# Optimization experiments

Hardware: AMD Instinct MI355X
Metric: run time of the kernel (lower is better)

The kernel has to match this reference:

```python
import jax, jax.numpy as jnp
import numpy as np
import math

# model / graph sizes
N_NODES, N_EDGES = 50000, 400000
IN_DIM, N_HID = 256, 128
NUM_TYPES, NUM_REL = 4, 5
N_HEADS, D_K = 4, 32
N_LAYERS, MAX_LEN = 2, 240
SQRT_DK = math.sqrt(D_K)


def _gelu(x):
    return jax.nn.gelu(x, approximate=False)  # torch F.gelu is exact erf


def _per_type_linear(x, types, W, b):
    # x:[n,din], types:[n] int, W:[T,din,dout], b:[T,dout]
    out = jnp.zeros((x.shape[0], W.shape[-1]), x.dtype)
    for t in range(W.shape[0]):  # small fixed type count
        out = jnp.where((types == t)[:, None], x @ W[t] + b[t], out)
    return out


def setup_inputs() -> dict:
    key = jax.random.key(0)
    ks = jax.random.split(key, 16)
    node_feature = jax.random.normal(ks[0], (N_NODES, IN_DIM), jnp.float32)
    node_type = jax.random.randint(ks[1], (N_NODES,), 0, NUM_TYPES)
    edge_index = jax.random.randint(ks[2], (2, N_EDGES), 0, N_NODES)
    edge_type = jax.random.randint(ks[3], (N_EDGES,), 0, NUM_REL)
    edge_time = jax.random.randint(ks[4], (N_EDGES,), 0, MAX_LEN)

    def w(k, shape, s=0.05):
        return jax.random.normal(k, shape, jnp.float32) * s

    adapt_W = w(ks[5], (NUM_TYPES, IN_DIM, N_HID))
    adapt_b = jnp.zeros((NUM_TYPES, N_HID), jnp.float32)
    Wk = w(ks[6], (N_LAYERS, NUM_TYPES, N_HID, N_HID))
    Wq = w(ks[7], (N_LAYERS, NUM_TYPES, N_HID, N_HID))
    Wv = w(ks[8], (N_LAYERS, NUM_TYPES, N_HID, N_HID))
    Wa = w(ks[9], (N_LAYERS, NUM_TYPES, N_HID, N_HID))
    bk = jnp.zeros((N_LAYERS, NUM_TYPES, N_HID), jnp.float32)
    bq = jnp.zeros((N_LAYERS, NUM_TYPES, N_HID), jnp.float32)
    bv = jnp.zeros((N_LAYERS, NUM_TYPES, N_HID), jnp.float32)
    ba = jnp.zeros((N_LAYERS, NUM_TYPES, N_HID), jnp.float32)
    rel_pri = jnp.ones((N_LAYERS, NUM_REL, N_HEADS), jnp.float32)
    rel_att = w(ks[10], (N_LAYERS, NUM_REL, N_HEADS, D_K, D_K), 0.1) + jnp.eye(D_K, dtype=jnp.float32)
    rel_msg = w(ks[11], (N_LAYERS, NUM_REL, N_HEADS, D_K, D_K), 0.1) + jnp.eye(D_K, dtype=jnp.float32)
    skip = jnp.ones((N_LAYERS, NUM_TYPES), jnp.float32)
    # fixed sinusoidal RTE table (pyHGT RelTemporalEncoding, requires_grad=False)
    pos = np.arange(MAX_LEN, dtype=np.float32)[:, None]
    div = np.exp(np.arange(0, N_HID, 2, dtype=np.float32) * -(math.log(10000.0) / N_HID))
    tab = np.zeros((MAX_LEN, N_HID), np.float32)
    tab[:, 0::2] = np.sin(pos * div) / math.sqrt(N_HID)
    tab[:, 1::2] = np.cos(pos * div) / math.sqrt(N_HID)
    rte_emb = jnp.asarray(tab)
    rte_W = w(ks[12], (N_LAYERS, N_HID, N_HID))
    rte_b = jnp.zeros((N_LAYERS, N_HID), jnp.float32)
    return dict(node_feature=node_feature, adapt_W=adapt_W, adapt_b=adapt_b,
                Wk=Wk, bk=bk, Wq=Wq, bq=bq, Wv=Wv, bv=bv, Wa=Wa, ba=ba,
                rel_pri=rel_pri, rel_att=rel_att, rel_msg=rel_msg, skip=skip,
                rte_emb=rte_emb, rte_W=rte_W, rte_b=rte_b,
                node_type=node_type, edge_index=edge_index,
                edge_type=edge_type, edge_time=edge_time)


def reference(node_feature, adapt_W, adapt_b, Wk, bk, Wq, bq, Wv, bv, Wa, ba,
              rel_pri, rel_att, rel_msg, skip, rte_emb, rte_W, rte_b,
              node_type, edge_index, edge_type, edge_time):
    n = node_feature.shape[0]
    src, dst = edge_index[0], edge_index[1]  # PyG: row0 = source j, row1 = target i
    st, tt = node_type[src], node_type[dst]
    # per-type input adaptation (all types use Linear + GELU)
    h = _gelu(_per_type_linear(node_feature, node_type, adapt_W, adapt_b))  # [N, n_hid]
    for l in range(N_LAYERS):  # HGTConv stack
        x_j, x_i = h[src], h[dst]
        s_e = x_j + rte_emb[edge_time] @ rte_W[l] + rte_b[l]  # RTE on source per edge
        k = _per_type_linear(s_e, st, Wk[l], bk[l]).reshape(-1, N_HEADS, D_K)
        v = _per_type_linear(s_e, st, Wv[l], bv[l]).reshape(-1, N_HEADS, D_K)
        q = _per_type_linear(x_i, tt, Wq[l], bq[l]).reshape(-1, N_HEADS, D_K)
        att = jnp.zeros((k.shape[0], N_HEADS), h.dtype)
        msg = jnp.zeros_like(v)
        for r in range(NUM_REL):  # small fixed relation count
            m = edge_type == r
            kr = jnp.einsum('ehd,hdk->ehk', k, rel_att[l, r])
            ar = jnp.einsum('ehd,ehd->eh', q, kr) * rel_pri[l, r] / SQRT_DK
            mr = jnp.einsum('ehd,hdk->ehk', v, rel_msg[l, r])
            att = jnp.where(m[:, None], ar, att)
            msg = jnp.where(m[:, None, None], mr, msg)
        # segment softmax over incoming edges of each target node
        amax = jax.lax.stop_gradient(jax.ops.segment_max(att, dst, num_segments=n))
        ex = jnp.exp(att - amax[dst])
        denom = jax.ops.segment_sum(ex, dst, num_segments=n)
        alpha = ex / (denom[dst] + 1e-16)
        aggr = jax.ops.segment_sum((msg * alpha[:, :, None]).reshape(-1, N_HEADS * D_K),
                                   dst, num_segments=n)  # [N, n_hid]
        g = _gelu(aggr)
        res = jnp.zeros_like(h)
        for t in range(NUM_TYPES):  # per-type output transform + gated skip
            a_t = jax.nn.sigmoid(skip[l, t])
            res = jnp.where((node_type == t)[:, None],
                            (g @ Wa[l, t] + ba[l, t]) * a_t + h * (1.0 - a_t), res)
        h = res
    return h
```

## Files before the change

### kernel.cpp

```cpp
#include <hip/hip_runtime.h>
#include <math.h>

#define NN     50000
#define NE     400000
#define INDIM  256
#define NH     128
#define NTYPE  4
#define NREL   5
#define NHEAD  4
#define DK     32
#define RSQRT_DK 0.17677669529663687f
#define BN     64
#define NSCAN_BLK ((NN + 255) / 256)
#define XB     260

__device__ __forceinline__ float gelu_f(float x){
    return 0.5f * x * (1.0f + erff(x * 0.70710678118654752f));
}

__global__ void GNN_nscatter(const int* __restrict__ ntype, int* __restrict__ ncur,
                             int* __restrict__ nperm){
    __shared__ int lcnt[4], lbase[4];
    int tid = threadIdx.x;
    if (tid < 4) lcnt[tid] = 0;
    __syncthreads();
    int n = blockIdx.x * 256 + tid;
    int t = 0, lpos = 0;
    bool ok = (n < NN);
    if (ok){ t = ntype[n]; lpos = atomicAdd(&lcnt[t], 1); }
    __syncthreads();
    if (tid < 4 && lcnt[tid] > 0) lbase[tid] = atomicAdd(&ncur[tid], lcnt[tid]);
    __syncthreads();
    if (ok) nperm[t * NN + lbase[t] + lpos] = n;
}

__global__ void GNN_deg(const int* __restrict__ edst, int* __restrict__ deg){
    int e = blockIdx.x * 256 + threadIdx.x;
    if (e < NE) atomicAdd(&deg[edst[e]], 1);
}

__global__ void GNN_scan1(const int* __restrict__ deg, int* __restrict__ rowptr,
                          int* __restrict__ bsum){
    __shared__ int s[256];
    int g = blockIdx.x * 256 + threadIdx.x;
    int v = (g < NN) ? deg[g] : 0;
    s[threadIdx.x] = v;
    __syncthreads();
    for (int off = 1; off < 256; off <<= 1){
        int t = (threadIdx.x >= off) ? s[threadIdx.x - off] : 0;
        __syncthreads();
        s[threadIdx.x] += t;
        __syncthreads();
    }
    if (g < NN) rowptr[g] = s[threadIdx.x] - v;
    if (threadIdx.x == 255) bsum[blockIdx.x] = s[255];
}

__global__ void GNN_scan2(const int* __restrict__ bsum, int* __restrict__ bbase){
    __shared__ int s[256];
    int v = (threadIdx.x < NSCAN_BLK) ? bsum[threadIdx.x] : 0;
    s[threadIdx.x] = v;
    __syncthreads();
    for (int off = 1; off < 256; off <<= 1){
        int t = (threadIdx.x >= off) ? s[threadIdx.x - off] : 0;
        __syncthreads();
        s[threadIdx.x] += t;
        __syncthreads();
    }
    bbase[threadIdx.x] = s[threadIdx.x] - v;
}

__global__ void GNN_scan3(int* __restrict__ rowptr, const int* __restrict__ bbase){
    int g = blockIdx.x * 256 + threadIdx.x;
    if (g < NN) rowptr[g] += bbase[blockIdx.x];
    if (g == 0) rowptr[NN] = NE;
}

__global__ void GNN_csr_scatter(const int* __restrict__ edst, const int* __restrict__ rowptr,
                                int* __restrict__ cursor, int* __restrict__ csr_e){
    int e = blockIdx.x * 256 + threadIdx.x;
    if (e >= NE) return;
    int d = edst[e];
    int pos = atomicAdd(&cursor[d], 1);
    csr_e[rowptr[d] + pos] = e;
}

template<int MODE>
__device__ __forceinline__ void gemm_tile(
    const float* __restrict__ X, int K,
    const float* __restrict__ W, const float* __restrict__ brow,
    float a_t, const float* __restrict__ Hprev,
    float* Xs, float* Ws, const int* nids,
    float* __restrict__ OUT)
{
    int tid = threadIdx.x;
    int cq = tid & 31, rq = tid >> 5;
    float acc[8][4];
    #pragma unroll
    for (int i = 0; i < 8; i++){ acc[i][0]=0.f; acc[i][1]=0.f; acc[i][2]=0.f; acc[i][3]=0.f; }

    for (int k0 = 0; k0 < K; k0 += 32){
        #pragma unroll
        for (int j = 0; j < 2; j++){
            int slot = j * 256 + tid;
            int c4 = slot >> 6, row = slot & 63;
            int nid = nids[row];
            float4 xv = make_float4(0.f, 0.f, 0.f, 0.f);
            if (nid >= 0) xv = *(const float4*)(X + (size_t)nid * K + k0 + c4 * 4);
            *(float4*)&Xs[c4 * XB + row * 4] = xv;
        }
        #pragma unroll
        for (int j = 0; j < 4; j++){
            int slot = j * 256 + tid;
            int kk = slot >> 5, col4 = slot & 31;
            *(float4*)&Ws[kk * 128 + col4 * 4] =
                *(const float4*)(W + (size_t)(k0 + kk) * NH + col4 * 4);
        }
        __syncthreads();
        #pragma unroll 2
        for (int c4 = 0; c4 < 8; c4++){
            float4 w0 = *(const float4*)&Ws[(c4*4+0)*128 + cq*4];
            float4 w1 = *(const float4*)&Ws[(c4*4+1)*128 + cq*4];
            float4 w2 = *(const float4*)&Ws[(c4*4+2)*128 + cq*4];
            float4 w3 = *(const float4*)&Ws[(c4*4+3)*128 + cq*4];
            #pragma unroll
            for (int i = 0; i < 8; i++){
                float4 xv = *(const float4*)&Xs[c4 * XB + (rq + 8*i) * 4];
                acc[i][0] += xv.x*w0.x + xv.y*w1.x + xv.z*w2.x + xv.w*w3.x;
                acc[i][1] += xv.x*w0.y + xv.y*w1.y + xv.z*w2.y + xv.w*w3.y;
                acc[i][2] += xv.x*w0.z + xv.y*w1.z + xv.z*w2.z + xv.w*w3.z;
                acc[i][3] += xv.x*w0.w + xv.y*w1.w + xv.z*w2.w + xv.w*w3.w;
            }
        }
        __syncthreads();
    }

    float4 b4 = *(const float4*)(brow + cq * 4);
    float one_m = 1.f - a_t;
    #pragma unroll
    for (int i = 0; i < 8; i++){
        int r = rq + 8*i;
        int nid = nids[r];
        if (nid < 0) continue;
        float v0 = acc[i][0] + b4.x, v1 = acc[i][1] + b4.y;
        float v2 = acc[i][2] + b4.z, v3 = acc[i][3] + b4.w;
        if (MODE == 0){ v0 = gelu_f(v0); v1 = gelu_f(v1); v2 = gelu_f(v2); v3 = gelu_f(v3); }
        if (MODE == 2){
            float4 hp = *(const float4*)(Hprev + (size_t)nid * NH + cq * 4);
            v0 = v0 * a_t + hp.x * one_m; v1 = v1 * a_t + hp.y * one_m;
            v2 = v2 * a_t + hp.z * one_m; v3 = v3 * a_t + hp.w * one_m;
        }
        *(float4*)(OUT + (size_t)nid * NH + cq * 4) = make_float4(v0, v1, v2, v3);
    }
}

template<int MODE>
__global__ __launch_bounds__(256) void GNN_ptype_gemm(
    const float* __restrict__ X, int K,
    const float* __restrict__ Wall, const float* __restrict__ ball,
    const float* __restrict__ skiprow, const float* __restrict__ Hprev,
    const int* __restrict__ nperm, const int* __restrict__ counts,
    float* __restrict__ OUT)
{
    int t = blockIdx.y;
    int cnt = counts[t];
    int rbase = blockIdx.x * BN;
    if (rbase >= cnt) return;
    __shared__ float Xs[8 * XB];
    __shared__ float Ws[32 * 128];
    __shared__ int nids[BN];
    int tid = threadIdx.x;
    if (tid < BN){
        int idx = rbase + tid;
        nids[tid] = (idx < cnt) ? nperm[t * NN + idx] : -1;
    }
    __syncthreads();
    float a_t = 0.f;
    if (MODE == 2) a_t = 1.f / (1.f + expf(-skiprow[t]));
    gemm_tile<MODE>(X, K, Wall + (size_t)t * K * NH, ball + t * NH,
                    a_t, Hprev, Xs, Ws, nids, OUT);
}

__global__ __launch_bounds__(256) void GNN_qkv_gemm(
    const float* __restrict__ X,
    const float* __restrict__ Wq, const float* __restrict__ bq,
    const float* __restrict__ Wk, const float* __restrict__ bk,
    const float* __restrict__ Wv, const float* __restrict__ bv,
    const int* __restrict__ nperm, const int* __restrict__ counts,
    float* __restrict__ Qn, float* __restrict__ Kn, float* __restrict__ Vn)
{
    int t = blockIdx.y;
    int cnt = counts[t];
    int rbase = blockIdx.x * BN;
    if (rbase >= cnt) return;
    __shared__ float Xs[8 * XB];
    __shared__ float Ws[32 * 128];
    __shared__ int nids[BN];
    int tid = threadIdx.x;
    if (tid < BN){
        int idx = rbase + tid;
        nids[tid] = (idx < cnt) ? nperm[t * NN + idx] : -1;
    }
    __syncthreads();
    int z = blockIdx.z;
    const float* W = (z == 0) ? Wq : (z == 1) ? Wk : Wv;
    const float* b = (z == 0) ? bq : (z == 1) ? bk : bv;
    float* OUT     = (z == 0) ? Qn : (z == 1) ? Kn : Vn;
    gemm_tile<1>(X, NH, W + (size_t)t * NH * NH, b + t * NH,
                 0.f, nullptr, Xs, Ws, nids, OUT);
}

__global__ void GNN_rte_tab(const float* __restrict__ rte_emb, const float* __restrict__ rW,
                            const float* __restrict__ rb, float* __restrict__ tab){
    int m = blockIdx.x, j = threadIdx.x;
    __shared__ float e[NH];
    e[j] = rte_emb[m * NH + j];
    __syncthreads();
    float a = rb[j];
    #pragma unroll 8
    for (int d = 0; d < NH; d++) a += e[d] * rW[d * NH + j];
    tab[m * NH + j] = a;
}

__global__ void GNN_rte_proj(const float* __restrict__ tab, const float* __restrict__ WkL,
                             const float* __restrict__ WvL, float* __restrict__ RK,
                             float* __restrict__ RV){
    int m = blockIdx.x, j = threadIdx.x;
    int sel = blockIdx.y; int t = sel >> 1; int which = sel & 1;
    const float* W = (which ? WvL : WkL) + (size_t)t * NH * NH;
    float* O = which ? RV : RK;
    __shared__ float e[NH];
    e[j] = tab[m * NH + j];
    __syncthreads();
    float a = 0.f;
    #pragma unroll 8
    for (int d = 0; d < NH; d++) a += e[d] * W[d * NH + j];
    O[(size_t)(t * 240 + m) * NH + j] = a;
}

__global__ __launch_bounds__(256) void GNN_qa(
    const float* __restrict__ Qn, const float* __restrict__ relA, float* __restrict__ QA)
{
    __shared__ float Atp[4 * 1072];
    int r = blockIdx.y;
    int nb = blockIdx.x * 64;
    int tid = threadIdx.x;
    const float* Ar = relA + (size_t)r * NHEAD * DK * DK;
    for (int x = tid; x < NHEAD * DK * DK; x += 256){
        int hh = x >> 10, rem = x & 1023, dd = rem >> 5, cc = rem & 31;
        Atp[hh * 1072 + (dd >> 2) * 132 + cc * 4 + (dd & 3)] = Ar[x];
    }
    __syncthreads();
    int cq = tid & 31, rq = tid >> 5;
    int h = cq >> 3;
    int abase = h * 1072 + (cq & 7) * 132;
    int rowoff[8];
    #pragma unroll
    for (int i = 0; i < 8; i++){
        int node = nb + rq + 8*i;
        if (node >= NN) node = NN - 1;
        rowoff[i] = node * NH + h * 32;
    }
    float acc[8][4];
    #pragma unroll
    for (int i = 0; i < 8; i++){ acc[i][0]=0.f; acc[i][1]=0.f; acc[i][2]=0.f; acc[i][3]=0.f; }
    #pragma unroll 2
    for (int c4 = 0; c4 < 8; c4++){
        float4 av0 = *(const float4*)&Atp[abase + c4 * 16 + 0];
        float4 av1 = *(const float4*)&Atp[abase + c4 * 16 + 4];
        float4 av2 = *(const float4*)&Atp[abase + c4 * 16 + 8];
        float4 av3 = *(const float4*)&Atp[abase + c4 * 16 + 12];
        #pragma unroll
        for (int i = 0; i < 8; i++){
            float4 qv = *(const float4*)(Qn + rowoff[i] + c4 * 4);
            acc[i][0] += qv.x*av0.x + qv.y*av1.x + qv.z*av2.x + qv.w*av3.x;
            acc[i][1] += qv.x*av0.y + qv.y*av1.y + qv.z*av2.y + qv.w*av3.y;
            acc[i][2] += qv.x*av0.z + qv.y*av1.z + qv.z*av2.z + qv.w*av3.z;
            acc[i][3] += qv.x*av0.w + qv.y*av1.w + qv.z*av2.w + qv.w*av3.w;
        }
    }
    #pragma unroll
    for (int i = 0; i < 8; i++){
        int node = nb + rq + 8*i;
        if (node >= NN) continue;
        *(float4*)(QA + ((size_t)r * NN + node) * NH + cq * 4) =
            make_float4(acc[i][0], acc[i][1], acc[i][2], acc[i][3]);
    }
}

__global__ __launch_bounds__(256) void GNN_edge_att(
    const float* __restrict__ Kn, const float* __restrict__ RK, const float* __restrict__ QA,
    const int* __restrict__ esrc, const int* __restrict__ edst,
    const int* __restrict__ etype, const int* __restrict__ etime,
    const int* __restrict__ ntype, const float* __restrict__ relP,
    float* __restrict__ att)
{
    int tid = threadIdx.x;
    int e = blockIdx.x * 8 + (tid >> 5);
    if (e >= NE) return;
    int lane = tid & 31;
    int s = esrc[e], d = edst[e], r = etype[e], tm = etime[e];
    int st = ntype[s];
    float4 k4 = *(const float4*)(Kn + (size_t)s * NH + lane * 4);
    float4 rk = *(const float4*)(RK + (size_t)(st * 240 + tm) * NH + lane * 4);
    float4 qa = *(const float4*)(QA + ((size_t)r * NN + d) * NH + lane * 4);
    float pv = (k4.x + rk.x) * qa.x + (k4.y + rk.y) * qa.y
             + (k4.z + rk.z) * qa.z + (k4.w + rk.w) * qa.w;
    pv += __shfl_xor(pv, 4);
    pv += __shfl_xor(pv, 2);
    pv += __shfl_xor(pv, 1);
    if ((lane & 7) == 0){
        int head = lane >> 3;
        att[(size_t)e * NHEAD + head] = pv * relP[r * NHEAD + head] * RSQRT_DK;
    }
}

__global__ __launch_bounds__(256) void GNN_node_aggr(
    const float* __restrict__ att, const float* __restrict__ Vn, const float* __restrict__ RV,
    const int* __restrict__ rowptr, const int* __restrict__ csr_e,
    const int* __restrict__ esrc, const int* __restrict__ etype,
    const int* __restrict__ etime, const int* __restrict__ ntype,
    float* __restrict__ P)
{
    int tid = threadIdx.x;
    int i = blockIdx.x * 8 + (tid >> 5);
    if (i >= NN) return;
    int lane = tid & 31;
    int head = lane >> 3;
    int beg = rowptr[i], end = rowptr[i + 1];
    float mx = -3.4e38f;
    for (int k = beg; k < end; k++){
        int e = csr_e[k];
        mx = fmaxf(mx, att[(size_t)e * NHEAD + head]);
    }
    float4 acc[NREL];
    #pragma unroll
    for (int rr = 0; rr < NREL; rr++) acc[rr] = make_float4(0.f, 0.f, 0.f, 0.f);
    float den = 0.f;
    for (int k = beg; k < end; k++){
        int e = csr_e[k];
        int s = esrc[e], r = etype[e], tm = etime[e];
        int st = ntype[s];
        float ex = expf(att[(size_t)e * NHEAD + head] - mx);
        den += ex;
        float4 v4 = *(const float4*)(Vn + (size_t)s * NH + lane * 4);
        float4 rv = *(const float4*)(RV + (size_t)(st * 240 + tm) * NH + lane * 4);
        float vx = v4.x + rv.x, vy = v4.y + rv.y, vz = v4.z + rv.z, vw = v4.w + rv.w;
        #pragma unroll
        for (int rr = 0; rr < NREL; rr++){
            float w = (rr == r) ? ex : 0.f;
            acc[rr].x += w * vx; acc[rr].y += w * vy;
            acc[rr].z += w * vz; acc[rr].w += w * vw;
        }
    }
    float inv = 1.f / (den + 1e-16f);
    #pragma unroll
    for (int rr = 0; rr < NREL; rr++){
        *(float4*)(P + ((size_t)rr * NN + i) * NH + lane * 4) =
            make_float4(acc[rr].x * inv, acc[rr].y * inv, acc[rr].z * inv, acc[rr].w * inv);
    }
}

__global__ __launch_bounds__(256) void GNN_pm(
    const float* __restrict__ P, const float* __restrict__ relM, float* __restrict__ aggr)
{
    __shared__ float Msp[2][4 * 1072];
    int tid = threadIdx.x;
    int nb = blockIdx.x * 64;
    int cq = tid & 31, rq = tid >> 5;
    int h = cq >> 3;
    int mbase = h * 1072 + (cq & 7) * 132;
    int rowoff[8];
    #pragma unroll
    for (int i = 0; i < 8; i++){
        int node = nb + rq + 8*i;
        if (node >= NN) node = NN - 1;
        rowoff[i] = node * NH + h * 32;
    }
    float acc[8][4];
    #pragma unroll
    for (int i = 0; i < 8; i++){ acc[i][0]=0.f; acc[i][1]=0.f; acc[i][2]=0.f; acc[i][3]=0.f; }

    #pragma unroll
    for (int j = 0; j < 4; j++){
        int s = tid + 256 * j;
        float4 mv = *(const float4*)(relM + 4 * s);
        *(float4*)&Msp[0][(s >> 8) * 1072 + (s & 7) * 132 + ((s >> 3) & 31) * 4] = mv;
    }
    __syncthreads();

    #pragma unroll
    for (int r = 0; r < NREL; r++){
        float4 mpre[4];
        if (r + 1 < NREL){
            const float* Mn = relM + (size_t)(r + 1) * NHEAD * DK * DK;
            #pragma unroll
            for (int j = 0; j < 4; j++)
                mpre[j] = *(const float4*)(Mn + 4 * (tid + 256 * j));
        }
        const float* Ms = Msp[r & 1];
        const float* Pr = P + (size_t)r * NN * NH;
        #pragma unroll 2
        for (int d4 = 0; d4 < 8; d4++){
            float4 mv0 = *(const float4*)&Ms[mbase + d4 * 16 + 0];
            float4 mv1 = *(const float4*)&Ms[mbase + d4 * 16 + 4];
            float4 mv2 = *(const float4*)&Ms[mbase + d4 * 16 + 8];
            float4 mv3 = *(const float4*)&Ms[mbase + d4 * 16 + 12];
            #pragma unroll
            for (int i = 0; i < 8; i++){
                float4 pv = *(const float4*)(Pr + rowoff[i] + d4 * 4);
                acc[i][0] += pv.x*mv0.x + pv.y*mv1.x + pv.z*mv2.x + pv.w*mv3.x;
                acc[i][1] += pv.x*mv0.y + pv.y*mv1.y + pv.z*mv2.y + pv.w*mv3.y;
                acc[i][2] += pv.x*mv0.z + pv.y*mv1.z + pv.z*mv2.z + pv.w*mv3.z;
                acc[i][3] += pv.x*mv0.w + pv.y*mv1.w + pv.z*mv2.w + pv.w*mv3.w;
            }
        }
        if (r + 1 < NREL){
            #pragma unroll
            for (int j = 0; j < 4; j++){
                int s = tid + 256 * j;
                *(float4*)&Msp[(r + 1) & 1][(s >> 8) * 1072 + (s & 7) * 132 +
                                            ((s >> 3) & 31) * 4] = mpre[j];
            }
            __syncthreads();
        }
    }
    #pragma unroll
    for (int i = 0; i < 8; i++){
        int node = nb + rq + 8*i;
        if (node >= NN) continue;
        *(float4*)(aggr + (size_t)node * NH + cq * 4) =
            make_float4(gelu_f(acc[i][0]), gelu_f(acc[i][1]),
                        gelu_f(acc[i][2]), gelu_f(acc[i][3]));
    }
}

extern "C" void kernel_launch(void* const* d_in, const int* in_sizes, int n_in,
                              void* d_out, int out_size, void* d_ws, size_t ws_size,
                              hipStream_t stream)
{
    const float* node_feature = (const float*)d_in[0];
    const float* adapt_W = (const float*)d_in[1];
    const float* adapt_b = (const float*)d_in[2];
    const float* Wk = (const float*)d_in[3];
    const float* bk = (const float*)d_in[4];
    const float* Wq = (const float*)d_in[5];
    const float* bq = (const float*)d_in[6];
    const float* Wv = (const float*)d_in[7];
    const float* bv = (const float*)d_in[8];
    const float* Wa = (const float*)d_in[9];
    const float* ba = (const float*)d_in[10];
    const float* rel_pri = (const float*)d_in[11];
    const float* rel_att = (const float*)d_in[12];
    const float* rel_msg = (const float*)d_in[13];
    const float* skip = (const float*)d_in[14];
    const float* rte_emb = (const float*)d_in[15];
    const float* rte_W = (const float*)d_in[16];
    const float* rte_b = (const float*)d_in[17];
    const int* node_type = (const int*)d_in[18];
    const int* edge_index = (const int*)d_in[19];
    const int* edge_type = (const int*)d_in[20];
    const int* edge_time = (const int*)d_in[21];
    const int* esrc = edge_index;
    const int* edst = edge_index + NE;

    char* p = (char*)d_ws;
    auto alloc = [&](size_t bytes) -> char* {
        char* r = p; p += (bytes + 255) & ~(size_t)255; return r;
    };
    float* hA    = (float*)alloc((size_t)NN * NH * 4);
    float* Qn    = (float*)alloc((size_t)NN * NH * 4);
    float* Kn    = (float*)alloc((size_t)NN * NH * 4);
    float* Vn    = (float*)alloc((size_t)NN * NH * 4);
    float* QA    = (float*)alloc((size_t)NREL * NN * NH * 4);
    float* rtab  = (float*)alloc((size_t)240 * NH * 4);
    float* RK    = (float*)alloc((size_t)NTYPE * 240 * NH * 4);
    float* RV    = (float*)alloc((size_t)NTYPE * 240 * NH * 4);
    int* nperm   = (int*)alloc((size_t)NTYPE * NN * 4);
    int* rowptr  = (int*)alloc((size_t)(NN + 1) * 4);
    int* csr_e   = (int*)alloc((size_t)NE * 4);
    int* deg     = (int*)alloc((size_t)2 * NN * 4);
    int* cursor  = deg + NN;
    int* bsum    = (int*)alloc(256 * 4);
    int* bbase   = (int*)alloc(256 * 4);
    int* ncur    = (int*)alloc(64);
    float* att   = Qn;
    float* Pbuf  = QA;
    float* aggr  = Kn;

    hipMemsetAsync(ncur, 0, 64, stream);
    hipMemsetAsync(deg, 0, (size_t)2 * NN * 4, stream);

    GNN_nscatter<<<(NN + 255) / 256, 256, 0, stream>>>(node_type, ncur, nperm);
    GNN_deg<<<(NE + 255) / 256, 256, 0, stream>>>(edst, deg);
    GNN_scan1<<<NSCAN_BLK, 256, 0, stream>>>(deg, rowptr, bsum);
    GNN_scan2<<<1, 256, 0, stream>>>(bsum, bbase);
    GNN_scan3<<<NSCAN_BLK, 256, 0, stream>>>(rowptr, bbase);
    GNN_csr_scatter<<<(NE + 255) / 256, 256, 0, stream>>>(edst, rowptr, cursor, csr_e);

    dim3 ggrid((NN + BN - 1) / BN, NTYPE);
    GNN_ptype_gemm<0><<<ggrid, 256, 0, stream>>>(node_feature, INDIM, adapt_W, adapt_b,
                                                 nullptr, nullptr, nperm, ncur, hA);
    const float* hin = hA;
    for (int l = 0; l < 2; l++){
        const float* WkL = Wk + (size_t)l * NTYPE * NH * NH;
        const float* WqL = Wq + (size_t)l * NTYPE * NH * NH;
        const float* WvL = Wv + (size_t)l * NTYPE * NH * NH;
        const float* WaL = Wa + (size_t)l * NTYPE * NH * NH;
        const float* bkL = bk + (size_t)l * NTYPE * NH;
        const float* bqL = bq + (size_t)l * NTYPE * NH;
        const float* bvL = bv + (size_t)l * NTYPE * NH;
        const float* baL = ba + (size_t)l * NTYPE * NH;
        const float* relA = rel_att + (size_t)l * NREL * NHEAD * DK * DK;
        const float* relM = rel_msg + (size_t)l * NREL * NHEAD * DK * DK;
        const float* relP = rel_pri + (size_t)l * NREL * NHEAD;

        GNN_rte_tab<<<240, 128, 0, stream>>>(rte_emb, rte_W + (size_t)l * NH * NH,
                                             rte_b + (size_t)l * NH, rtab);
        GNN_rte_proj<<<dim3(240, NTYPE * 2), 128, 0, stream>>>(rtab, WkL, WvL, RK, RV);

        GNN_qkv_gemm<<<dim3(ggrid.x, NTYPE, 3), 256, 0, stream>>>(
            hin, WqL, bqL, WkL, bkL, WvL, bvL, nperm, ncur, Qn, Kn, Vn);

        GNN_qa<<<dim3((NN + 63) / 64, NREL), 256, 0, stream>>>(Qn, relA, QA);

        GNN_edge_att<<<(NE + 7) / 8, 256, 0, stream>>>(
            Kn, RK, QA, esrc, edst, edge_type, edge_time, node_type, relP, att);

        GNN_node_aggr<<<(NN + 7) / 8, 256, 0, stream>>>(
            att, Vn, RV, rowptr, csr_e, esrc, edge_type, edge_time, node_type, Pbuf);

        GNN_pm<<<(NN + 63) / 64, 256, 0, stream>>>(Pbuf, relM, aggr);

        float* hout = (l == 0) ? hA : (float*)d_out;
        GNN_ptype_gemm<2><<<ggrid, 256, 0, stream>>>(
            aggr, NH, WaL, baL, skip + (size_t)l * NTYPE, hin,
            nperm, ncur, hout);
        hin = hout;
    }
}
```

Measured before the change: 1.133 ms.

## Split per-type GEMM into column halves with direct X loads and double-buffered W

Each per-type GEMM block now computes only 64 of the 128 output columns, so the grid doubles in x and more blocks run concurrently. X rows are read straight from global memory into registers instead of being staged in shared memory. The weight tile is double-buffered in shared memory, with the next tile prefetched into registers, which removes one barrier per k-step. In exchange, every X row is fetched by both column halves, and the X gathers are no longer staged for reuse, so the kernel leans more on cache behaviour.

```diff
diff --git a/kernel.cpp b/kernel.cpp
--- a/kernel.cpp
+++ b/kernel.cpp
@@ -12,7 +12,6 @@
 #define RSQRT_DK 0.17677669529663687f
 #define BN     64
 #define NSCAN_BLK ((NN + 255) / 256)
-#define XB     260
 
 __device__ __forceinline__ float gelu_f(float x){
     return 0.5f * x * (1.0f + erff(x * 0.70710678118654752f));
@@ -86,71 +85,91 @@
 }
 
 template<int MODE>
-__device__ __forceinline__ void gemm_tile(
+__device__ __forceinline__ void gemm_tile64(
     const float* __restrict__ X, int K,
-    const float* __restrict__ W, const float* __restrict__ brow,
+    const float* __restrict__ W,
+    const float* __restrict__ brow,
     float a_t, const float* __restrict__ Hprev,
-    float* Xs, float* Ws, const int* nids,
+    float (*Ws)[2048], const int* nids, int half,
     float* __restrict__ OUT)
 {
     int tid = threadIdx.x;
-    int cq = tid & 31, rq = tid >> 5;
-    float acc[8][4];
-    #pragma unroll
-    for (int i = 0; i < 8; i++){ acc[i][0]=0.f; acc[i][1]=0.f; acc[i][2]=0.f; acc[i][3]=0.f; }
-
+    int cq = tid & 15, rq = tid >> 4;
+    int co = half * 64 + cq * 4;
+    int wk0 = tid >> 4, wc = (tid & 15) * 4;
+
+    int nA = nids[rq], nB = nids[rq + 16], nC = nids[rq + 32], nD = nids[rq + 48];
+    const float* xpA = X + (size_t)(nA < 0 ? 0 : nA) * K;
+    const float* xpB = X + (size_t)(nB < 0 ? 0 : nB) * K;
+    const float* xpC = X + (size_t)(nC < 0 ? 0 : nC) * K;
+    const float* xpD = X + (size_t)(nD < 0 ? 0 : nD) * K;
+
+    float4 wr0, wr1;
+    #define LOADW(k0)                                                           \
+        wr0 = *(const float4*)(W + (size_t)((k0) + wk0     ) * NH + half*64 + wc); \
+        wr1 = *(const float4*)(W + (size_t)((k0) + wk0 + 16) * NH + half*64 + wc);
+    #define WRITEW(b)                                                           \
+        *(float4*)&Ws[b][(wk0     ) * 64 + wc] = wr0;                           \
+        *(float4*)&Ws[b][(wk0 + 16) * 64 + wc] = wr1;
+
+    float acc[4][4];
+    #pragma unroll
+    for (int i = 0; i < 4; i++){ acc[i][0]=0.f; acc[i][1]=0.f; acc[i][2]=0.f; acc[i][3]=0.f; }
+
+    LOADW(0);
+    int buf = 0;
     for (int k0 = 0; k0 < K; k0 += 32){
-        #pragma unroll
-        for (int j = 0; j < 2; j++){
-            int slot = j * 256 + tid;
-            int c4 = slot >> 6, row = slot & 63;
-            int nid = nids[row];
-            float4 xv = make_float4(0.f, 0.f, 0.f, 0.f);
-            if (nid >= 0) xv = *(const float4*)(X + (size_t)nid * K + k0 + c4 * 4);
-            *(float4*)&Xs[c4 * XB + row * 4] = xv;
-        }
-        #pragma unroll
-        for (int j = 0; j < 4; j++){
-            int slot = j * 256 + tid;
-            int kk = slot >> 5, col4 = slot & 31;
-            *(float4*)&Ws[kk * 128 + col4 * 4] =
-                *(const float4*)(W + (size_t)(k0 + kk) * NH + col4 * 4);
-        }
+        WRITEW(buf);
         __syncthreads();
+        if (k0 + 32 < K){ LOADW(k0 + 32); }
         #pragma unroll 2
         for (int c4 = 0; c4 < 8; c4++){
-            float4 w0 = *(const float4*)&Ws[(c4*4+0)*128 + cq*4];
-            float4 w1 = *(const float4*)&Ws[(c4*4+1)*128 + cq*4];
-            float4 w2 = *(const float4*)&Ws[(c4*4+2)*128 + cq*4];
-            float4 w3 = *(const float4*)&Ws[(c4*4+3)*128 + cq*4];
-            #pragma unroll
-            for (int i = 0; i < 8; i++){
-                float4 xv = *(const float4*)&Xs[c4 * XB + (rq + 8*i) * 4];
-                acc[i][0] += xv.x*w0.x + xv.y*w1.x + xv.z*w2.x + xv.w*w3.x;
-                acc[i][1] += xv.x*w0.y + xv.y*w1.y + xv.z*w2.y + xv.w*w3.y;
-                acc[i][2] += xv.x*w0.z + xv.y*w1.z + xv.z*w2.z + xv.w*w3.z;
-                acc[i][3] += xv.x*w0.w + xv.y*w1.w + xv.z*w2.w + xv.w*w3.w;
-            }
-        }
-        __syncthreads();
-    }
-
-    float4 b4 = *(const float4*)(brow + cq * 4);
+            float4 w0 = *(const float4*)&Ws[buf][(c4*4+0)*64 + cq*4];
+            float4 w1 = *(const float4*)&Ws[buf][(c4*4+1)*64 + cq*4];
+            float4 w2 = *(const float4*)&Ws[buf][(c4*4+2)*64 + cq*4];
+            float4 w3 = *(const float4*)&Ws[buf][(c4*4+3)*64 + cq*4];
+            float4 xA = *(const float4*)(xpA + k0 + c4*4);
+            float4 xB = *(const float4*)(xpB + k0 + c4*4);
+            float4 xC = *(const float4*)(xpC + k0 + c4*4);
+            float4 xD = *(const float4*)(xpD + k0 + c4*4);
+            acc[0][0] += xA.x*w0.x + xA.y*w1.x + xA.z*w2.x + xA.w*w3.x;
+            acc[0][1] += xA.x*w0.y + xA.y*w1.y + xA.z*w2.y + xA.w*w3.y;
+            acc[0][2] += xA.x*w0.z + xA.y*w1.z + xA.z*w2.z + xA.w*w3.z;
+            acc[0][3] += xA.x*w0.w + xA.y*w1.w + xA.z*w2.w + xA.w*w3.w;
+            acc[1][0] += xB.x*w0.x + xB.y*w1.x + xB.z*w2.x + xB.w*w3.x;
+            acc[1][1] += xB.x*w0.y + xB.y*w1.y + xB.z*w2.y + xB.w*w3.y;
+            acc[1][2] += xB.x*w0.z + xB.y*w1.z + xB.z*w2.z + xB.w*w3.z;
+            acc[1][3] += xB.x*w0.w + xB.y*w1.w + xB.z*w2.w + xB.w*w3.w;
+            acc[2][0] += xC.x*w0.x + xC.y*w1.x + xC.z*w2.x + xC.w*w3.x;
+            acc[2][1] += xC.x*w0.y + xC.y*w1.y + xC.z*w2.y + xC.w*w3.y;
+            acc[2][2] += xC.x*w0.z + xC.y*w1.z + xC.z*w2.z + xC.w*w3.z;
+            acc[2][3] += xC.x*w0.w + xC.y*w1.w + xC.z*w2.w + xC.w*w3.w;
+            acc[3][0] += xD.x*w0.x + xD.y*w1.x + xD.z*w2.x + xD.w*w3.x;
+            acc[3][1] += xD.x*w0.y + xD.y*w1.y + xD.z*w2.y + xD.w*w3.y;
+            acc[3][2] += xD.x*w0.z + xD.y*w1.z + xD.z*w2.z + xD.w*w3.z;
+            acc[3][3] += xD.x*w0.w + xD.y*w1.w + xD.z*w2.w + xD.w*w3.w;
+        }
+        buf ^= 1;
+    }
+    #undef LOADW
+    #undef WRITEW
+
+    float4 b4 = *(const float4*)(brow + co);
     float one_m = 1.f - a_t;
-    #pragma unroll
-    for (int i = 0; i < 8; i++){
-        int r = rq + 8*i;
-        int nid = nids[r];
+    int nid4[4] = {nA, nB, nC, nD};
+    #pragma unroll
+    for (int i = 0; i < 4; i++){
+        int nid = nid4[i];
         if (nid < 0) continue;
         float v0 = acc[i][0] + b4.x, v1 = acc[i][1] + b4.y;
         float v2 = acc[i][2] + b4.z, v3 = acc[i][3] + b4.w;
         if (MODE == 0){ v0 = gelu_f(v0); v1 = gelu_f(v1); v2 = gelu_f(v2); v3 = gelu_f(v3); }
         if (MODE == 2){
-            float4 hp = *(const float4*)(Hprev + (size_t)nid * NH + cq * 4);
+            float4 hp = *(const float4*)(Hprev + (size_t)nid * NH + co);
             v0 = v0 * a_t + hp.x * one_m; v1 = v1 * a_t + hp.y * one_m;
             v2 = v2 * a_t + hp.z * one_m; v3 = v3 * a_t + hp.w * one_m;
         }
-        *(float4*)(OUT + (size_t)nid * NH + cq * 4) = make_float4(v0, v1, v2, v3);
+        *(float4*)(OUT + (size_t)nid * NH + co) = make_float4(v0, v1, v2, v3);
     }
 }
 
@@ -164,10 +183,11 @@
 {
     int t = blockIdx.y;
     int cnt = counts[t];
-    int rbase = blockIdx.x * BN;
+    int bx = blockIdx.x;
+    int half = bx & 1;
+    int rbase = (bx >> 1) * BN;
     if (rbase >= cnt) return;
-    __shared__ float Xs[8 * XB];
-    __shared__ float Ws[32 * 128];
+    __shared__ float Ws[2][2048];
     __shared__ int nids[BN];
     int tid = threadIdx.x;
     if (tid < BN){
@@ -177,8 +197,8 @@
     __syncthreads();
     float a_t = 0.f;
     if (MODE == 2) a_t = 1.f / (1.f + expf(-skiprow[t]));
-    gemm_tile<MODE>(X, K, Wall + (size_t)t * K * NH, ball + t * NH,
-                    a_t, Hprev, Xs, Ws, nids, OUT);
+    gemm_tile64<MODE>(X, K, Wall + (size_t)t * K * NH, ball + t * NH,
+                      a_t, Hprev, Ws, nids, half, OUT);
 }
 
 __global__ __launch_bounds__(256) void GNN_qkv_gemm(
@@ -191,10 +211,11 @@
 {
     int t = blockIdx.y;
     int cnt = counts[t];
-    int rbase = blockIdx.x * BN;
+    int bx = blockIdx.x;
+    int half = bx & 1;
+    int rbase = (bx >> 1) * BN;
     if (rbase >= cnt) return;
-    __shared__ float Xs[8 * XB];
-    __shared__ float Ws[32 * 128];
+    __shared__ float Ws[2][2048];
     __shared__ int nids[BN];
     int tid = threadIdx.x;
     if (tid < BN){
@@ -206,8 +227,8 @@
     const float* W = (z == 0) ? Wq : (z == 1) ? Wk : Wv;
     const float* b = (z == 0) ? bq : (z == 1) ? bk : bv;
     float* OUT     = (z == 0) ? Qn : (z == 1) ? Kn : Vn;
-    gemm_tile<1>(X, NH, W + (size_t)t * NH * NH, b + t * NH,
-                 0.f, nullptr, Xs, Ws, nids, OUT);
+    gemm_tile64<1>(X, NH, W + (size_t)t * NH * NH, b + t * NH,
+                   0.f, nullptr, Ws, nids, half, OUT);
 }
 
 __global__ void GNN_rte_tab(const float* __restrict__ rte_emb, const float* __restrict__ rW,
@@ -498,7 +519,7 @@
     GNN_scan3<<<NSCAN_BLK, 256, 0, stream>>>(rowptr, bbase);
     GNN_csr_scatter<<<(NE + 255) / 256, 256, 0, stream>>>(edst, rowptr, cursor, csr_e);
 
-    dim3 ggrid((NN + BN - 1) / BN, NTYPE);
+    dim3 ggrid(((NN + BN - 1) / BN) * 2, NTYPE);
     GNN_ptype_gemm<0><<<ggrid, 256, 0, stream>>>(node_feature, INDIM, adapt_W, adapt_b,
                                                  nullptr, nullptr, nperm, ncur, hA);
     const float* hin = hA;
```

Result: slower. 1.157 ms (+2.1%).
